# Optimization experiments

Measured on AMD Instinct MI355X. Metric: run time of the kernel, lower is better.

The kernel has to match this reference:

```python
import jax, jax.numpy as jnp
import numpy as np

D_MODEL = 1024
NUM_HEADS = 16
HEAD_DIM = D_MODEL // NUM_HEADS
THETA = 10000.0
MAX_SEQ_LEN = 2048
BATCH = 4
SEQ = 2048


def _rope_tables():
    # theta_vec = 1 / theta**(arange(0, d_k, 2)/d_k), pos outer product
    inv_freq = 1.0 / (THETA ** (jnp.arange(0, HEAD_DIM, 2, dtype=jnp.float32) / HEAD_DIM))
    pos = jnp.arange(MAX_SEQ_LEN, dtype=jnp.float32)
    freqs = jnp.outer(pos, inv_freq)  # [max_seq, head_dim//2]
    return jnp.cos(freqs), jnp.sin(freqs)


def apply_rope(x, cos, sin):
    # x: [..., S, d]; cos/sin: [S, d//2]; interleaved pairwise rotation
    x1 = x[..., 0::2]
    x2 = x[..., 1::2]
    o1 = x1 * cos - x2 * sin
    o2 = x2 * cos + x1 * sin
    return jnp.stack([o1, o2], axis=-1).reshape(x.shape)


def setup_inputs() -> dict:
    key = jax.random.key(0)
    kx, kq, kk, kv, ko = jax.random.split(key, 5)
    std = (1.0 / D_MODEL) ** 0.5
    x = jax.random.normal(kx, (BATCH, SEQ, D_MODEL), dtype=jnp.float32)
    w_q = jax.random.normal(kq, (D_MODEL, D_MODEL), dtype=jnp.float32) * std
    w_k = jax.random.normal(kk, (D_MODEL, D_MODEL), dtype=jnp.float32) * std
    w_v = jax.random.normal(kv, (D_MODEL, D_MODEL), dtype=jnp.float32) * std
    w_o = jax.random.normal(ko, (D_MODEL, D_MODEL), dtype=jnp.float32) * std
    cos, sin = _rope_tables()
    return {"x": x, "w_q": w_q, "w_k": w_k, "w_v": w_v, "w_o": w_o,
            "cos": cos, "sin": sin}


def reference(x, w_q, w_k, w_v, w_o, cos, sin):
    b, s, d = x.shape
    h, dk = NUM_HEADS, HEAD_DIM

    def proj(w):
        # einsum '... s d, hd d -> ... s hd' == x @ w.T, then split heads
        y = jnp.einsum('bsd,ed->bse', x, w)
        return y.reshape(b, s, h, dk).transpose(0, 2, 1, 3)  # [b,h,s,dk]

    q = apply_rope(proj(w_q), cos[:s], sin[:s])
    k = apply_rope(proj(w_k), cos[:s], sin[:s])
    v = proj(w_v)

    scores = jnp.einsum('bhnd,bhmd->bhnm', q, k) / (dk ** 0.5)
    causal = jnp.tril(jnp.ones((s, s), dtype=bool))
    scores = jnp.where(causal, scores, -jnp.inf)
    attn = jax.nn.softmax(scores, axis=-1)
    out = jnp.einsum('bhnm,bhmd->bhnd', attn, v)  # [b,h,s,dk]
    out = out.transpose(0, 2, 1, 3).reshape(b, s, d)
    # einsum '... s hd, d hd -> ... s d' == out @ w_o.T
    return jnp.einsum('bse,de->bsd', out, w_o)
```

## Files before the change

### kernel.cpp

```cpp
#include <hip/hip_runtime.h>
#include <hip/hip_bf16.h>


typedef __bf16 bf16;
typedef __bf16 bf16x8 __attribute__((ext_vector_type(8)));
typedef __bf16 bf16x4 __attribute__((ext_vector_type(4)));
typedef float f32x4 __attribute__((ext_vector_type(4)));

#define LOG2E 1.4426950408889634f
#define QSCALE (0.125f * LOG2E * 8388608.0f)
#define SEXP_SEED ((126.94269504f - 16.0f * LOG2E) * 8388608.0f)

__device__ __forceinline__ void async16(const void* g, void* l) {
  __builtin_amdgcn_global_load_lds(
      (const __attribute__((address_space(1))) void*)g,
      (__attribute__((address_space(3))) void*)l, 16, 0, 0);
}

#define MFMA16(a, b, c) __builtin_amdgcn_mfma_f32_16x16x32_bf16(a, b, c, 0, 0, 0)

__global__ void cast_all_kernel(const float* __restrict__ x,
                                const float* __restrict__ wq,
                                const float* __restrict__ wk,
                                const float* __restrict__ wv,
                                const float* __restrict__ wo,
                                bf16* __restrict__ xb, bf16* __restrict__ wb) {
  int i = blockIdx.x * blockDim.x + threadIdx.x;
  const float* src;
  bf16* dst;
  long o;
  if (i < 2097152) {
    src = x; dst = xb; o = i;
  } else {
    long j = i - 2097152;
    int w = (int)(j >> 18);
    o = j & 262143;
    src = (w == 0) ? wq : (w == 1) ? wk : (w == 2) ? wv : wo;
    dst = wb + (long)w * 1048576;
  }
  float4 v = reinterpret_cast<const float4*>(src)[o];
  bf16x4 out;
  out.x = (bf16)v.x; out.y = (bf16)v.y; out.z = (bf16)v.z; out.w = (bf16)v.w;
  *reinterpret_cast<bf16x4*>(dst + o * 4) = out;
}

template <int EPI, int TM, int TN>
__global__ __launch_bounds__(256) void gemm_tile(const bf16* __restrict__ A,
                                                 const bf16* __restrict__ B,
                                                 void* __restrict__ C, int N,
                                                 int K) {
  constexpr int WM = TM / 64;
  constexpr int WN = 4 / WM;
  constexpr int CW = TN / WN;
  constexpr int NT = CW / 16;
  constexpr int ROUNDS = (TM + TN) / 64;
  __shared__ __align__(16) bf16 As[TM * 32];
  __shared__ __align__(16) bf16 Bs[TN * 32];
  const int tid = threadIdx.x;
  const int wid = tid >> 6, lane = tid & 63;
  const int quad = lane >> 4, l15 = lane & 15;
  const int waveM = wid / WN, waveN = wid % WN;
  const int bm = blockIdx.y, bn = blockIdx.x;

  f32x4 acc[4][NT] = {};

  const bf16* Ag = A + (long)bm * TM * K;
  const bf16* Bg = B + (long)bn * TN * K;

  for (int k0 = 0; k0 < K; k0 += 32) {
#pragma unroll
    for (int ri = 0; ri < ROUNDS; ++ri) {
      int c = ri * 256 + tid;
      int g = ri * 256 + (wid << 6);
      bool isA = g < TM * 4;
      int cl = isA ? c : c - TM * 4;
      int r = cl >> 2;
      int col = ((cl & 3) ^ (r & 3)) << 3;
      const bf16* src = (isA ? Ag : Bg) + (long)r * K + k0 + col;
      char* dst = isA ? ((char*)As + (long)g * 16)
                      : ((char*)Bs + (long)(g - TM * 4) * 16);
      async16(src, dst);
    }
    __syncthreads();
    bf16x8 af[4], bfr[NT];
#pragma unroll
    for (int t = 0; t < 4; ++t) {
      int rowA = waveM * 64 + t * 16 + l15;
      af[t] = *(const bf16x8*)(As + rowA * 32 + ((quad ^ (rowA & 3)) << 3));
    }
#pragma unroll
    for (int t = 0; t < NT; ++t) {
      int rowB = waveN * CW + t * 16 + l15;
      bfr[t] = *(const bf16x8*)(Bs + rowB * 32 + ((quad ^ (rowB & 3)) << 3));
    }
#pragma unroll
    for (int mt = 0; mt < 4; ++mt)
#pragma unroll
      for (int nt = 0; nt < NT; ++nt)
        acc[mt][nt] = MFMA16(af[mt], bfr[nt], acc[mt][nt]);
    __syncthreads();
  }

#pragma unroll
  for (int mt = 0; mt < 4; ++mt)
#pragma unroll
    for (int nt = 0; nt < NT; ++nt)
#pragma unroll
      for (int r = 0; r < 4; ++r) {
        int row = bm * TM + waveM * 64 + mt * 16 + quad * 4 + r;
        int col = bn * TN + waveN * CW + nt * 16 + l15;
        float v = acc[mt][nt][r];
        if (EPI == 1) {
          long off = (long)(col >> 11) * 2097152 + (long)row * 2048 +
                     (col & 2047);
          ((bf16*)C)[off] = (bf16)v;
        } else {
          ((float*)C)[(long)row * N + col] = v;
        }
      }
}

__global__ __launch_bounds__(256) void gemm_qk(const bf16* __restrict__ A,
                                               const bf16* __restrict__ B,
                                               bf16* __restrict__ QK,
                                               const float* __restrict__ cosT,
                                               const float* __restrict__ sinT,
                                               int K) {
  __shared__ __align__(16) bf16 As[128 * 32];
  __shared__ __align__(16) bf16 Bs[128 * 32];
  const int tid = threadIdx.x;
  const int wid = tid >> 6, lane = tid & 63;
  const int quad = lane >> 4, l15 = lane & 15;
  const int waveM = wid >> 1, waveN = wid & 1;
  const int bm = blockIdx.y, bn = blockIdx.x;

  f32x4 acc[4][4] = {};
  const bf16* Ag = A + (long)bm * 128 * K;
  const bf16* Bg = B + (long)bn * 128 * K;

  for (int k0 = 0; k0 < K; k0 += 32) {
#pragma unroll
    for (int it = 0; it < 2; ++it) {
      int chunk = it * 256 + tid;
      int r = chunk >> 2;
      int c = ((chunk & 3) ^ (r & 3)) << 3;
      int ldsbase = (it * 256 + wid * 64) * 16;
      async16(Ag + (long)r * K + k0 + c, (char*)As + ldsbase);
      async16(Bg + (long)r * K + k0 + c, (char*)Bs + ldsbase);
    }
    __syncthreads();
    bf16x8 af[4], bfr[4];
#pragma unroll
    for (int t = 0; t < 4; ++t) {
      int rowA = waveM * 64 + t * 16 + l15;
      af[t] = *(const bf16x8*)(As + rowA * 32 + ((quad ^ (rowA & 3)) << 3));
    }
#pragma unroll
    for (int t = 0; t < 4; ++t) {
      int rowB = waveN * 64 + t * 16 + l15;
      bfr[t] = *(const bf16x8*)(Bs + rowB * 32 + ((quad ^ (rowB & 3)) << 3));
    }
#pragma unroll
    for (int mt = 0; mt < 4; ++mt)
#pragma unroll
      for (int nt = 0; nt < 4; ++nt)
        acc[mt][nt] = MFMA16(af[mt], bfr[nt], acc[mt][nt]);
    __syncthreads();
  }

  const float qsc = (bn < 8) ? QSCALE : 1.0f;
#pragma unroll
  for (int mt = 0; mt < 4; ++mt)
#pragma unroll
    for (int nt = 0; nt < 4; ++nt)
#pragma unroll
      for (int r = 0; r < 4; ++r) {
        int row = bm * 128 + waveM * 64 + mt * 16 + quad * 4 + r;
        int col = bn * 128 + waveN * 64 + nt * 16 + l15;
        float v = acc[mt][nt][r];
        float pr = __shfl_xor(v, 1);
        int d = col & 63;
        int ti = (row & 2047) * 32 + (d >> 1);
        float c = cosT[ti], sn = sinT[ti];
        float o = (col & 1) ? (v * c + pr * sn) : (v * c - pr * sn);
        o *= qsc;
        long off = (long)(col >> 10) * 8388608 +
                   (long)(((row >> 11) << 4) + ((col >> 6) & 15)) * 131072 +
                   (long)(row & 2047) * 64 + d;
        QK[off] = (bf16)o;
      }
}

__device__ __forceinline__ void attn_step(const bf16* Ks, const bf16* Vs,
                                          bf16* Pw, const bf16x8* qf,
                                          const bf16x8 ones, f32x4* accO,
                                          f32x4& accL, int quad, int l15,
                                          int qloc, bool diag) {
  const int sw = l15 & 7;
  const f32x4 seedv = {SEXP_SEED, SEXP_SEED, SEXP_SEED, SEXP_SEED};
  f32x4 sacc[4] = {seedv, seedv, seedv, seedv};
#pragma unroll
  for (int mt = 0; mt < 4; ++mt)
#pragma unroll
    for (int kk = 0; kk < 2; ++kk) {
      bf16x8 kf = *(const bf16x8*)(Ks + (mt * 16 + l15) * 64 +
                                   ((((kk << 2) + quad) ^ sw) << 3));
      sacc[mt] = MFMA16(kf, qf[kk], sacc[mt]);
    }
  if (diag) {
#pragma unroll
    for (int mt = 0; mt < 4; ++mt)
#pragma unroll
      for (int r = 0; r < 4; ++r)
        if ((mt * 16 + quad * 4 + r) > qloc) sacc[mt][r] = 0.0f;
  }
#pragma unroll
  for (int mt = 0; mt < 4; ++mt) {
    int i0 = (int)sacc[mt][0], i1 = (int)sacc[mt][1];
    int i2 = (int)sacc[mt][2], i3 = (int)sacc[mt][3];
    uint2 pk;
    pk.x = __builtin_amdgcn_perm((unsigned)i1, (unsigned)i0, 0x07060302u);
    pk.y = __builtin_amdgcn_perm((unsigned)i3, (unsigned)i2, 0x07060302u);
    *(uint2*)(Pw + l15 * 88 + mt * 16 + quad * 4) = pk;
  }
  asm volatile("s_waitcnt lgkmcnt(0)" ::: "memory");
  bf16x8 pfr[2];
#pragma unroll
  for (int kk = 0; kk < 2; ++kk)
    pfr[kk] = *(const bf16x8*)(Pw + l15 * 88 + kk * 32 + quad * 8);
#pragma unroll
  for (int nt = 0; nt < 4; ++nt)
#pragma unroll
    for (int kk = 0; kk < 2; ++kk) {
      bf16x8 vf = *(const bf16x8*)(Vs + (nt * 16 + l15) * 64 +
                                   ((((kk << 2) + quad) ^ sw) << 3));
      accO[nt] = MFMA16(pfr[kk], vf, accO[nt]);
    }
#pragma unroll
  for (int kk = 0; kk < 2; ++kk)
    accL = MFMA16(pfr[kk], ones, accL);
}

__global__ __launch_bounds__(256, 4) void attn_kernel(
    const bf16* __restrict__ Q, const bf16* __restrict__ Kg,
    const bf16* __restrict__ VT, bf16* __restrict__ Out) {
  __shared__ __align__(16) bf16 Ks[64 * 64];
  __shared__ __align__(16) bf16 Vs[64 * 64];
  __shared__ __align__(16) bf16 Ps[4][16 * 88];
  const int tid = threadIdx.x, wid = tid >> 6, lane = tid & 63;
  const int quad = lane >> 4, l15 = lane & 15;
  const int p = blockIdx.x, bh = blockIdx.y;
  const int q0t = p, q1t = 31 - p;
  const bf16* Qb = Q + (long)bh * 131072;
  const bf16* Kb = Kg + (long)bh * 131072;
  const bf16* Vb = VT + (long)bh * 131072;
  bf16* Pw = &Ps[wid][0];
  const int qloc = wid * 16 + l15;

  bf16x8 ones;
#pragma unroll
  for (int j = 0; j < 8; ++j) ones[j] = (bf16)1.0f;

  bf16x8 qf0[2], qf1[2];
#pragma unroll
  for (int kk = 0; kk < 2; ++kk) {
    qf0[kk] = *(const bf16x8*)(Qb + (long)(q0t * 64 + qloc) * 64 + kk * 32 +
                               quad * 8);
    qf1[kk] = *(const bf16x8*)(Qb + (long)(q1t * 64 + qloc) * 64 + kk * 32 +
                               quad * 8);
  }
  f32x4 acc0[4] = {}, acc1[4] = {};
  f32x4 accL0 = {}, accL1 = {};

  for (int kt = 0; kt <= q1t; ++kt) {
#pragma unroll
    for (int it = 0; it < 2; ++it) {
      int chunk = it * 256 + tid;
      int r = chunk >> 3;
      int c = (((chunk & 7) ^ (r & 7)) << 3);
      int ldsbase = (it * 256 + wid * 64) * 16;
      async16(Kb + (long)(kt * 64 + r) * 64 + c, (char*)Ks + ldsbase);
      async16(Vb + (long)r * 2048 + kt * 64 + c, (char*)Vs + ldsbase);
    }
    __syncthreads();
    attn_step(Ks, Vs, Pw, qf1, ones, acc1, accL1, quad, l15, qloc, kt == q1t);
    if (kt <= q0t)
      attn_step(Ks, Vs, Pw, qf0, ones, acc0, accL0, quad, l15, qloc,
                kt == q0t);
    __syncthreads();
  }

  const int b = bh >> 4, h = bh & 15;
#pragma unroll
  for (int r = 0; r < 4; ++r) {
    float lr0 = 1.0f / accL0[r];
    float lr1 = 1.0f / accL1[r];
#pragma unroll
    for (int nt = 0; nt < 4; ++nt) {
      int d = h * 64 + nt * 16 + l15;
      int qg0 = q0t * 64 + wid * 16 + quad * 4 + r;
      int qg1 = q1t * 64 + wid * 16 + quad * 4 + r;
      Out[(long)(b * 2048 + qg0) * 1024 + d] = (bf16)(acc0[nt][r] * lr0);
      Out[(long)(b * 2048 + qg1) * 1024 + d] = (bf16)(acc1[nt][r] * lr1);
    }
  }
}

extern "C" void kernel_launch(void* const* d_in, const int* in_sizes, int n_in,
                              void* d_out, int out_size, void* d_ws,
                              size_t ws_size, hipStream_t stream) {
  const float* x = (const float*)d_in[0];
  const float* w_q = (const float*)d_in[1];
  const float* w_k = (const float*)d_in[2];
  const float* w_v = (const float*)d_in[3];
  const float* w_o = (const float*)d_in[4];
  const float* cosT = (const float*)d_in[5];
  const float* sinT = (const float*)d_in[6];

  char* ws = (char*)d_ws;
  bf16* xb = (bf16*)(ws + 0);
  bf16* wqb = (bf16*)(ws + 16777216);
  bf16* wvb = (bf16*)(ws + 20971520);
  bf16* wob = (bf16*)(ws + 23068672);
  bf16* Qb = (bf16*)(ws + 25165824);
  bf16* Kb = (bf16*)(ws + 41943040);
  bf16* VTb = (bf16*)(ws + 58720256);
  bf16* attnb = xb;

  cast_all_kernel<<<12288, 256, 0, stream>>>(x, w_q, w_k, w_v, w_o, xb, wqb);

  gemm_qk<<<dim3(16, 64), 256, 0, stream>>>(xb, wqb, Qb, cosT, sinT, 1024);
  gemm_tile<1, 64, 128><<<dim3(64, 16), 256, 0, stream>>>(wvb, xb, VTb, 8192,
                                                          1024);

  attn_kernel<<<dim3(16, 64), 256, 0, stream>>>(Qb, Kb, VTb, attnb);

  gemm_tile<2, 128, 64><<<dim3(16, 64), 256, 0, stream>>>(attnb, wob,
                                                          (float*)d_out, 1024,
                                                          1024);
}
```

Before: 284.9 us.

## Interleave dual query tiles in attention loop and pack cos/sin table

The attention inner loop now handles both query tiles together. Each K and V fragment read from LDS feeds two MFMAs, and the two P buffers are separate, so the two dependency chains can interleave. The aim is fewer LDS reads and more instruction-level parallelism on the MFMA pipe, at the cost of more registers and doubled P scratch. Separately, the cast kernel interleaves the cos and sin tables into a float2 array so the RoPE epilogue does one load per element instead of two.

New measurement: 306.0 us. +7.4%, slower.

```diff
diff --git a/kernel.cpp b/kernel.cpp
--- a/kernel.cpp
+++ b/kernel.cpp
@@ -24,8 +24,19 @@
                                 const float* __restrict__ wk,
                                 const float* __restrict__ wv,
                                 const float* __restrict__ wo,
-                                bf16* __restrict__ xb, bf16* __restrict__ wb) {
+                                const float* __restrict__ cosT,
+                                const float* __restrict__ sinT,
+                                bf16* __restrict__ xb, bf16* __restrict__ wb,
+                                float2* __restrict__ csT) {
   int i = blockIdx.x * blockDim.x + threadIdx.x;
+  if (i >= 3145728) {
+    int j = i - 3145728;
+    float2 cs;
+    cs.x = cosT[j];
+    cs.y = sinT[j];
+    csT[j] = cs;
+    return;
+  }
   const float* src;
   bf16* dst;
   long o;
@@ -123,8 +134,7 @@
 __global__ __launch_bounds__(256) void gemm_qk(const bf16* __restrict__ A,
                                                const bf16* __restrict__ B,
                                                bf16* __restrict__ QK,
-                                               const float* __restrict__ cosT,
-                                               const float* __restrict__ sinT,
+                                               const float2* __restrict__ csT,
                                                int K) {
   __shared__ __align__(16) bf16 As[128 * 32];
   __shared__ __align__(16) bf16 Bs[128 * 32];
@@ -180,9 +190,8 @@
         float v = acc[mt][nt][r];
         float pr = __shfl_xor(v, 1);
         int d = col & 63;
-        int ti = (row & 2047) * 32 + (d >> 1);
-        float c = cosT[ti], sn = sinT[ti];
-        float o = (col & 1) ? (v * c + pr * sn) : (v * c - pr * sn);
+        float2 cs = csT[(row & 2047) * 32 + (d >> 1)];
+        float o = (col & 1) ? (v * cs.x + pr * cs.y) : (v * cs.x - pr * cs.y);
         o *= qsc;
         long off = (long)(col >> 10) * 8388608 +
                    (long)(((row >> 11) << 4) + ((col >> 6) & 15)) * 131072 +
@@ -191,62 +200,12 @@
       }
 }
 
-__device__ __forceinline__ void attn_step(const bf16* Ks, const bf16* Vs,
-                                          bf16* Pw, const bf16x8* qf,
-                                          const bf16x8 ones, f32x4* accO,
-                                          f32x4& accL, int quad, int l15,
-                                          int qloc, bool diag) {
-  const int sw = l15 & 7;
-  const f32x4 seedv = {SEXP_SEED, SEXP_SEED, SEXP_SEED, SEXP_SEED};
-  f32x4 sacc[4] = {seedv, seedv, seedv, seedv};
-#pragma unroll
-  for (int mt = 0; mt < 4; ++mt)
-#pragma unroll
-    for (int kk = 0; kk < 2; ++kk) {
-      bf16x8 kf = *(const bf16x8*)(Ks + (mt * 16 + l15) * 64 +
-                                   ((((kk << 2) + quad) ^ sw) << 3));
-      sacc[mt] = MFMA16(kf, qf[kk], sacc[mt]);
-    }
-  if (diag) {
-#pragma unroll
-    for (int mt = 0; mt < 4; ++mt)
-#pragma unroll
-      for (int r = 0; r < 4; ++r)
-        if ((mt * 16 + quad * 4 + r) > qloc) sacc[mt][r] = 0.0f;
-  }
-#pragma unroll
-  for (int mt = 0; mt < 4; ++mt) {
-    int i0 = (int)sacc[mt][0], i1 = (int)sacc[mt][1];
-    int i2 = (int)sacc[mt][2], i3 = (int)sacc[mt][3];
-    uint2 pk;
-    pk.x = __builtin_amdgcn_perm((unsigned)i1, (unsigned)i0, 0x07060302u);
-    pk.y = __builtin_amdgcn_perm((unsigned)i3, (unsigned)i2, 0x07060302u);
-    *(uint2*)(Pw + l15 * 88 + mt * 16 + quad * 4) = pk;
-  }
-  asm volatile("s_waitcnt lgkmcnt(0)" ::: "memory");
-  bf16x8 pfr[2];
-#pragma unroll
-  for (int kk = 0; kk < 2; ++kk)
-    pfr[kk] = *(const bf16x8*)(Pw + l15 * 88 + kk * 32 + quad * 8);
-#pragma unroll
-  for (int nt = 0; nt < 4; ++nt)
-#pragma unroll
-    for (int kk = 0; kk < 2; ++kk) {
-      bf16x8 vf = *(const bf16x8*)(Vs + (nt * 16 + l15) * 64 +
-                                   ((((kk << 2) + quad) ^ sw) << 3));
-      accO[nt] = MFMA16(pfr[kk], vf, accO[nt]);
-    }
-#pragma unroll
-  for (int kk = 0; kk < 2; ++kk)
-    accL = MFMA16(pfr[kk], ones, accL);
-}
-
 __global__ __launch_bounds__(256, 4) void attn_kernel(
     const bf16* __restrict__ Q, const bf16* __restrict__ Kg,
     const bf16* __restrict__ VT, bf16* __restrict__ Out) {
   __shared__ __align__(16) bf16 Ks[64 * 64];
   __shared__ __align__(16) bf16 Vs[64 * 64];
-  __shared__ __align__(16) bf16 Ps[4][16 * 88];
+  __shared__ __align__(16) bf16 Ps[4][2][16 * 88];
   const int tid = threadIdx.x, wid = tid >> 6, lane = tid & 63;
   const int quad = lane >> 4, l15 = lane & 15;
   const int p = blockIdx.x, bh = blockIdx.y;
@@ -254,8 +213,10 @@
   const bf16* Qb = Q + (long)bh * 131072;
   const bf16* Kb = Kg + (long)bh * 131072;
   const bf16* Vb = VT + (long)bh * 131072;
-  bf16* Pw = &Ps[wid][0];
+  bf16* Pw1 = &Ps[wid][0][0];
+  bf16* Pw0 = &Ps[wid][1][0];
   const int qloc = wid * 16 + l15;
+  const int sw = l15 & 7;
 
   bf16x8 ones;
 #pragma unroll
@@ -271,6 +232,7 @@
   }
   f32x4 acc0[4] = {}, acc1[4] = {};
   f32x4 accL0 = {}, accL1 = {};
+  const f32x4 seedv = {SEXP_SEED, SEXP_SEED, SEXP_SEED, SEXP_SEED};
 
   for (int kt = 0; kt <= q1t; ++kt) {
 #pragma unroll
@@ -283,10 +245,103 @@
       async16(Vb + (long)r * 2048 + kt * 64 + c, (char*)Vs + ldsbase);
     }
     __syncthreads();
-    attn_step(Ks, Vs, Pw, qf1, ones, acc1, accL1, quad, l15, qloc, kt == q1t);
-    if (kt <= q0t)
-      attn_step(Ks, Vs, Pw, qf0, ones, acc0, accL0, quad, l15, qloc,
-                kt == q0t);
+    const bool dual = (kt <= q0t);
+
+    f32x4 s1[4] = {seedv, seedv, seedv, seedv};
+    f32x4 s0[4] = {seedv, seedv, seedv, seedv};
+    if (dual) {
+#pragma unroll
+      for (int mt = 0; mt < 4; ++mt)
+#pragma unroll
+        for (int kk = 0; kk < 2; ++kk) {
+          bf16x8 kf = *(const bf16x8*)(Ks + (mt * 16 + l15) * 64 +
+                                       ((((kk << 2) + quad) ^ sw) << 3));
+          s1[mt] = MFMA16(kf, qf1[kk], s1[mt]);
+          s0[mt] = MFMA16(kf, qf0[kk], s0[mt]);
+        }
+    } else {
+#pragma unroll
+      for (int mt = 0; mt < 4; ++mt)
+#pragma unroll
+        for (int kk = 0; kk < 2; ++kk) {
+          bf16x8 kf = *(const bf16x8*)(Ks + (mt * 16 + l15) * 64 +
+                                       ((((kk << 2) + quad) ^ sw) << 3));
+          s1[mt] = MFMA16(kf, qf1[kk], s1[mt]);
+        }
+    }
+    if (kt == q1t) {
+#pragma unroll
+      for (int mt = 0; mt < 4; ++mt)
+#pragma unroll
+        for (int r = 0; r < 4; ++r)
+          if ((mt * 16 + quad * 4 + r) > qloc) s1[mt][r] = 0.0f;
+    }
+    if (dual && kt == q0t) {
+#pragma unroll
+      for (int mt = 0; mt < 4; ++mt)
+#pragma unroll
+        for (int r = 0; r < 4; ++r)
+          if ((mt * 16 + quad * 4 + r) > qloc) s0[mt][r] = 0.0f;
+    }
+
+#pragma unroll
+    for (int mt = 0; mt < 4; ++mt) {
+      int i0 = (int)s1[mt][0], i1 = (int)s1[mt][1];
+      int i2 = (int)s1[mt][2], i3 = (int)s1[mt][3];
+      uint2 pk;
+      pk.x = __builtin_amdgcn_perm((unsigned)i1, (unsigned)i0, 0x07060302u);
+      pk.y = __builtin_amdgcn_perm((unsigned)i3, (unsigned)i2, 0x07060302u);
+      *(uint2*)(Pw1 + l15 * 88 + mt * 16 + quad * 4) = pk;
+    }
+    if (dual) {
+#pragma unroll
+      for (int mt = 0; mt < 4; ++mt) {
+        int i0 = (int)s0[mt][0], i1 = (int)s0[mt][1];
+        int i2 = (int)s0[mt][2], i3 = (int)s0[mt][3];
+        uint2 pk;
+        pk.x = __builtin_amdgcn_perm((unsigned)i1, (unsigned)i0, 0x07060302u);
+        pk.y = __builtin_amdgcn_perm((unsigned)i3, (unsigned)i2, 0x07060302u);
+        *(uint2*)(Pw0 + l15 * 88 + mt * 16 + quad * 4) = pk;
+      }
+    }
+    asm volatile("s_waitcnt lgkmcnt(0)" ::: "memory");
+    bf16x8 pf1[2], pf0[2];
+#pragma unroll
+    for (int kk = 0; kk < 2; ++kk)
+      pf1[kk] = *(const bf16x8*)(Pw1 + l15 * 88 + kk * 32 + quad * 8);
+    if (dual) {
+#pragma unroll
+      for (int kk = 0; kk < 2; ++kk)
+        pf0[kk] = *(const bf16x8*)(Pw0 + l15 * 88 + kk * 32 + quad * 8);
+    }
+
+    if (dual) {
+#pragma unroll
+      for (int nt = 0; nt < 4; ++nt)
+#pragma unroll
+        for (int kk = 0; kk < 2; ++kk) {
+          bf16x8 vf = *(const bf16x8*)(Vs + (nt * 16 + l15) * 64 +
+                                       ((((kk << 2) + quad) ^ sw) << 3));
+          acc1[nt] = MFMA16(pf1[kk], vf, acc1[nt]);
+          acc0[nt] = MFMA16(pf0[kk], vf, acc0[nt]);
+        }
+#pragma unroll
+      for (int kk = 0; kk < 2; ++kk) {
+        accL1 = MFMA16(pf1[kk], ones, accL1);
+        accL0 = MFMA16(pf0[kk], ones, accL0);
+      }
+    } else {
+#pragma unroll
+      for (int nt = 0; nt < 4; ++nt)
+#pragma unroll
+        for (int kk = 0; kk < 2; ++kk) {
+          bf16x8 vf = *(const bf16x8*)(Vs + (nt * 16 + l15) * 64 +
+                                       ((((kk << 2) + quad) ^ sw) << 3));
+          acc1[nt] = MFMA16(pf1[kk], vf, acc1[nt]);
+        }
+#pragma unroll
+      for (int kk = 0; kk < 2; ++kk) accL1 = MFMA16(pf1[kk], ones, accL1);
+    }
     __syncthreads();
   }
 
@@ -325,11 +380,13 @@
   bf16* Qb = (bf16*)(ws + 25165824);
   bf16* Kb = (bf16*)(ws + 41943040);
   bf16* VTb = (bf16*)(ws + 58720256);
+  float2* csT = (float2*)(ws + 75497472);
   bf16* attnb = xb;
 
-  cast_all_kernel<<<12288, 256, 0, stream>>>(x, w_q, w_k, w_v, w_o, xb, wqb);
-
-  gemm_qk<<<dim3(16, 64), 256, 0, stream>>>(xb, wqb, Qb, cosT, sinT, 1024);
+  cast_all_kernel<<<12544, 256, 0, stream>>>(x, w_q, w_k, w_v, w_o, cosT,
+                                             sinT, xb, wqb, csT);
+
+  gemm_qk<<<dim3(16, 64), 256, 0, stream>>>(xb, wqb, Qb, csT, 1024);
   gemm_tile<1, 64, 128><<<dim3(64, 16), 256, 0, stream>>>(wvb, xb, VTb, 8192,
                                                           1024);
 
```

## Merge QK and V projection GEMMs into one launch with interleaved blocks

Applied to the files above, without the earlier changes.

The QK projection (with RoPE epilogue) and the transposed V projection now run in a single kernel. Even and odd blocks are interleaved so both GEMMs share one launch and fill the GPU together. The cos/sin tables are packed into one float2 table during the cast kernel, so each RoPE element needs one load instead of two. The LDS swizzle changes from row&3 to (row>>1)&3 to alter the bank-conflict pattern. The cost is an extra small packing pass and a larger merged grid, where the two halves have different tile shapes.

After: 294.1 us. 1.03x slower.

```diff
diff --git a/kernel.cpp b/kernel.cpp
--- a/kernel.cpp
+++ b/kernel.cpp
@@ -24,8 +24,19 @@
                                 const float* __restrict__ wk,
                                 const float* __restrict__ wv,
                                 const float* __restrict__ wo,
-                                bf16* __restrict__ xb, bf16* __restrict__ wb) {
+                                const float* __restrict__ cosT,
+                                const float* __restrict__ sinT,
+                                bf16* __restrict__ xb, bf16* __restrict__ wb,
+                                float2* __restrict__ csT) {
   int i = blockIdx.x * blockDim.x + threadIdx.x;
+  if (i >= 3145728) {
+    int j = i - 3145728;
+    float2 cs;
+    cs.x = cosT[j];
+    cs.y = sinT[j];
+    csT[j] = cs;
+    return;
+  }
   const float* src;
   bf16* dst;
   long o;
@@ -45,25 +56,22 @@
 }
 
 template <int EPI, int TM, int TN>
-__global__ __launch_bounds__(256) void gemm_tile(const bf16* __restrict__ A,
-                                                 const bf16* __restrict__ B,
-                                                 void* __restrict__ C, int N,
-                                                 int K) {
+__device__ __forceinline__ void gemm_dev(const bf16* __restrict__ A,
+                                         const bf16* __restrict__ B,
+                                         void* __restrict__ C, int N, int K,
+                                         int bm, int bn, bf16* As, bf16* Bs,
+                                         const float2* __restrict__ csT) {
   constexpr int WM = TM / 64;
   constexpr int WN = 4 / WM;
   constexpr int CW = TN / WN;
   constexpr int NT = CW / 16;
   constexpr int ROUNDS = (TM + TN) / 64;
-  __shared__ __align__(16) bf16 As[TM * 32];
-  __shared__ __align__(16) bf16 Bs[TN * 32];
   const int tid = threadIdx.x;
   const int wid = tid >> 6, lane = tid & 63;
   const int quad = lane >> 4, l15 = lane & 15;
   const int waveM = wid / WN, waveN = wid % WN;
-  const int bm = blockIdx.y, bn = blockIdx.x;
 
   f32x4 acc[4][NT] = {};
-
   const bf16* Ag = A + (long)bm * TM * K;
   const bf16* Bg = B + (long)bn * TN * K;
 
@@ -75,7 +83,7 @@
       bool isA = g < TM * 4;
       int cl = isA ? c : c - TM * 4;
       int r = cl >> 2;
-      int col = ((cl & 3) ^ (r & 3)) << 3;
+      int col = ((cl & 3) ^ ((r >> 1) & 3)) << 3;
       const bf16* src = (isA ? Ag : Bg) + (long)r * K + k0 + col;
       char* dst = isA ? ((char*)As + (long)g * 16)
                       : ((char*)Bs + (long)(g - TM * 4) * 16);
@@ -86,12 +94,14 @@
 #pragma unroll
     for (int t = 0; t < 4; ++t) {
       int rowA = waveM * 64 + t * 16 + l15;
-      af[t] = *(const bf16x8*)(As + rowA * 32 + ((quad ^ (rowA & 3)) << 3));
+      af[t] =
+          *(const bf16x8*)(As + rowA * 32 + ((quad ^ ((rowA >> 1) & 3)) << 3));
     }
 #pragma unroll
     for (int t = 0; t < NT; ++t) {
       int rowB = waveN * CW + t * 16 + l15;
-      bfr[t] = *(const bf16x8*)(Bs + rowB * 32 + ((quad ^ (rowB & 3)) << 3));
+      bfr[t] =
+          *(const bf16x8*)(Bs + rowB * 32 + ((quad ^ ((rowB >> 1) & 3)) << 3));
     }
 #pragma unroll
     for (int mt = 0; mt < 4; ++mt)
@@ -101,6 +111,7 @@
     __syncthreads();
   }
 
+  const float qsc = (EPI == 0 && bn < 8) ? QSCALE : 1.0f;
 #pragma unroll
   for (int mt = 0; mt < 4; ++mt)
 #pragma unroll
@@ -110,7 +121,18 @@
         int row = bm * TM + waveM * 64 + mt * 16 + quad * 4 + r;
         int col = bn * TN + waveN * CW + nt * 16 + l15;
         float v = acc[mt][nt][r];
-        if (EPI == 1) {
+        if (EPI == 0) {
+          float pr = __shfl_xor(v, 1);
+          int d = col & 63;
+          float2 cs = csT[(row & 2047) * 32 + (d >> 1)];
+          float o =
+              (col & 1) ? (v * cs.x + pr * cs.y) : (v * cs.x - pr * cs.y);
+          o *= qsc;
+          long off = (long)(col >> 10) * 8388608 +
+                     (long)(((row >> 11) << 4) + ((col >> 6) & 15)) * 131072 +
+                     (long)(row & 2047) * 64 + d;
+          ((bf16*)C)[off] = (bf16)o;
+        } else if (EPI == 1) {
           long off = (long)(col >> 11) * 2097152 + (long)row * 2048 +
                      (col & 2047);
           ((bf16*)C)[off] = (bf16)v;
@@ -120,75 +142,31 @@
       }
 }
 
-__global__ __launch_bounds__(256) void gemm_qk(const bf16* __restrict__ A,
-                                               const bf16* __restrict__ B,
-                                               bf16* __restrict__ QK,
-                                               const float* __restrict__ cosT,
-                                               const float* __restrict__ sinT,
-                                               int K) {
+__global__ __launch_bounds__(256) void gemm_qkv(const bf16* __restrict__ xb,
+                                                const bf16* __restrict__ wqk,
+                                                const bf16* __restrict__ wv,
+                                                bf16* __restrict__ QK,
+                                                bf16* __restrict__ VT,
+                                                const float2* __restrict__ csT) {
   __shared__ __align__(16) bf16 As[128 * 32];
   __shared__ __align__(16) bf16 Bs[128 * 32];
-  const int tid = threadIdx.x;
-  const int wid = tid >> 6, lane = tid & 63;
-  const int quad = lane >> 4, l15 = lane & 15;
-  const int waveM = wid >> 1, waveN = wid & 1;
-  const int bm = blockIdx.y, bn = blockIdx.x;
-
-  f32x4 acc[4][4] = {};
-  const bf16* Ag = A + (long)bm * 128 * K;
-  const bf16* Bg = B + (long)bn * 128 * K;
-
-  for (int k0 = 0; k0 < K; k0 += 32) {
-#pragma unroll
-    for (int it = 0; it < 2; ++it) {
-      int chunk = it * 256 + tid;
-      int r = chunk >> 2;
-      int c = ((chunk & 3) ^ (r & 3)) << 3;
-      int ldsbase = (it * 256 + wid * 64) * 16;
-      async16(Ag + (long)r * K + k0 + c, (char*)As + ldsbase);
-      async16(Bg + (long)r * K + k0 + c, (char*)Bs + ldsbase);
-    }
-    __syncthreads();
-    bf16x8 af[4], bfr[4];
-#pragma unroll
-    for (int t = 0; t < 4; ++t) {
-      int rowA = waveM * 64 + t * 16 + l15;
-      af[t] = *(const bf16x8*)(As + rowA * 32 + ((quad ^ (rowA & 3)) << 3));
-    }
-#pragma unroll
-    for (int t = 0; t < 4; ++t) {
-      int rowB = waveN * 64 + t * 16 + l15;
-      bfr[t] = *(const bf16x8*)(Bs + rowB * 32 + ((quad ^ (rowB & 3)) << 3));
-    }
-#pragma unroll
-    for (int mt = 0; mt < 4; ++mt)
-#pragma unroll
-      for (int nt = 0; nt < 4; ++nt)
-        acc[mt][nt] = MFMA16(af[mt], bfr[nt], acc[mt][nt]);
-    __syncthreads();
-  }
-
-  const float qsc = (bn < 8) ? QSCALE : 1.0f;
-#pragma unroll
-  for (int mt = 0; mt < 4; ++mt)
-#pragma unroll
-    for (int nt = 0; nt < 4; ++nt)
-#pragma unroll
-      for (int r = 0; r < 4; ++r) {
-        int row = bm * 128 + waveM * 64 + mt * 16 + quad * 4 + r;
-        int col = bn * 128 + waveN * 64 + nt * 16 + l15;
-        float v = acc[mt][nt][r];
-        float pr = __shfl_xor(v, 1);
-        int d = col & 63;
-        int ti = (row & 2047) * 32 + (d >> 1);
-        float c = cosT[ti], sn = sinT[ti];
-        float o = (col & 1) ? (v * c + pr * sn) : (v * c - pr * sn);
-        o *= qsc;
-        long off = (long)(col >> 10) * 8388608 +
-                   (long)(((row >> 11) << 4) + ((col >> 6) & 15)) * 131072 +
-                   (long)(row & 2047) * 64 + d;
-        QK[off] = (bf16)o;
-      }
+  int id = blockIdx.x >> 1;
+  if (blockIdx.x & 1) {
+    gemm_dev<1, 64, 128>(wv, xb, VT, 8192, 1024, id >> 6, id & 63, As, Bs,
+                         nullptr);
+  } else {
+    gemm_dev<0, 128, 128>(xb, wqk, QK, 2048, 1024, id >> 4, id & 15, As, Bs,
+                          csT);
+  }
+}
+
+__global__ __launch_bounds__(256) void gemm_out(const bf16* __restrict__ A,
+                                                const bf16* __restrict__ B,
+                                                float* __restrict__ C) {
+  __shared__ __align__(16) bf16 As[128 * 32];
+  __shared__ __align__(16) bf16 Bs[64 * 32];
+  gemm_dev<2, 128, 64>(A, B, C, 1024, 1024, blockIdx.y, blockIdx.x, As, Bs,
+                       nullptr);
 }
 
 __device__ __forceinline__ void attn_step(const bf16* Ks, const bf16* Vs,
@@ -325,17 +303,15 @@
   bf16* Qb = (bf16*)(ws + 25165824);
   bf16* Kb = (bf16*)(ws + 41943040);
   bf16* VTb = (bf16*)(ws + 58720256);
+  float2* csT = (float2*)(ws + 75497472);
   bf16* attnb = xb;
 
-  cast_all_kernel<<<12288, 256, 0, stream>>>(x, w_q, w_k, w_v, w_o, xb, wqb);
-
-  gemm_qk<<<dim3(16, 64), 256, 0, stream>>>(xb, wqb, Qb, cosT, sinT, 1024);
-  gemm_tile<1, 64, 128><<<dim3(64, 16), 256, 0, stream>>>(wvb, xb, VTb, 8192,
-                                                          1024);
+  cast_all_kernel<<<12544, 256, 0, stream>>>(x, w_q, w_k, w_v, w_o, cosT,
+                                             sinT, xb, wqb, csT);
+
+  gemm_qkv<<<2048, 256, 0, stream>>>(xb, wqb, wvb, Qb, VTb, csT);
 
   attn_kernel<<<dim3(16, 64), 256, 0, stream>>>(Qb, Kb, VTb, attnb);
 
-  gemm_tile<2, 128, 64><<<dim3(16, 64), 256, 0, stream>>>(attnb, wob,
-                                                          (float*)d_out, 1024,
-                                                          1024);
-}
+  gemm_out<<<dim3(16, 64), 256, 0, stream>>>(attnb, wob, (float*)d_out);
+}
```
